# Kernel optimization log

Hardware: AMD Instinct MI355X
Metric: run time of the kernel (lower is better)

The kernel has to match this reference:

```python
import jax, jax.numpy as jnp
import numpy as np

N_NODES = 100000
N_REL = 500
N_EDGES = 600000
DIM = 128


def setup_inputs() -> dict:
    key = jax.random.key(0)
    ks = jax.random.split(key, 10)
    ent = jax.random.normal(ks[0], (N_NODES, DIM), dtype=jnp.float32)
    rel = jax.random.normal(ks[1], (N_REL, DIM), dtype=jnp.float32)
    edge_index = jax.random.randint(ks[2], (2, N_EDGES), 0, N_NODES, dtype=jnp.int64)
    edge_type = jax.random.randint(ks[3], (N_EDGES,), 0, N_REL, dtype=jnp.int64)
    s = 1.0 / np.sqrt(DIM)
    W_self = jax.random.uniform(ks[4], (DIM, DIM), jnp.float32, -s, s)
    b_self = jax.random.uniform(ks[5], (DIM,), jnp.float32, -s, s)
    W_nei = jax.random.uniform(ks[6], (DIM, DIM), jnp.float32, -s, s)
    b_nei = jax.random.uniform(ks[7], (DIM,), jnp.float32, -s, s)
    W_rel = jax.random.uniform(ks[8], (DIM, DIM), jnp.float32, -s, s)
    b_rel = jax.random.uniform(ks[9], (DIM,), jnp.float32, -s, s)
    return {
        "ent": ent, "rel": rel, "edge_index": edge_index, "edge_type": edge_type,
        "W_self": W_self, "b_self": b_self,
        "W_nei": W_nei, "b_nei": b_nei,
        "W_rel": W_rel, "b_rel": b_rel,
    }


def reference(ent, rel, edge_index, edge_type, W_self, b_self, W_nei, b_nei, W_rel, b_rel):
    src, dst = edge_index[0], edge_index[1]
    # gather -> sigmoid-gate -> scatter-add
    msg = ent[src] * jax.nn.sigmoid(rel[edge_type])          # [E, dim]
    agg = jax.ops.segment_sum(msg, dst, num_segments=ent.shape[0])  # [N, dim]
    out_ent = jax.nn.relu(ent @ W_self.T + b_self + agg @ W_nei.T + b_nei)
    out_rel = rel @ W_rel.T + b_rel
    return (out_ent, out_rel)
```

## Files before the change

kernel.cpp:

```cpp
#include <hip/hip_runtime.h>
#include <hip/hip_bf16.h>
#include <math.h>

#define DIM 128

typedef __bf16 bf8 __attribute__((ext_vector_type(8)));
typedef float f4 __attribute__((ext_vector_type(4)));
typedef float f2 __attribute__((ext_vector_type(2)));

struct __align__(8) bf16x4 { __hip_bfloat162 a, b; };

__global__ __launch_bounds__(256) void prep_kernel(
    const float* __restrict__ rel,
    const float* __restrict__ Ws,
    const float* __restrict__ Wn,
    const float* __restrict__ Wr,
    __hip_bfloat16* __restrict__ sigb,
    __hip_bfloat16* __restrict__ Wcat,
    float* __restrict__ Wt_rel,
    int* __restrict__ offs,
    uint2* __restrict__ spack2,
    int nSig, int nSigTot, int sigBlocks, int N, int R,
    int zeroBlocks, int fillQuads) {
    int b = blockIdx.x;
    if (b < sigBlocks) {
        int i = b * 256 + threadIdx.x;
        if (i < nSigTot) {
            float v = 0.f;
            if (i < nSig) {
                float x = rel[i];
                v = 1.0f / (1.0f + expf(-x));
            }
            sigb[i] = __float2bfloat16(v);
        }
    } else if (b < sigBlocks + 32) {
        int idx = (b - sigBlocks) * 256 + threadIdx.x;
        int j  = idx >> 6;
        int k0 = (idx & 63) * 4;
        const float* src = (k0 < DIM) ? &Ws[j * DIM + k0] : &Wn[j * DIM + (k0 - DIM)];
        float4 v = *(const float4*)src;
        bf16x4 o;
        o.a.x = __float2bfloat16(v.x);
        o.a.y = __float2bfloat16(v.y);
        o.b.x = __float2bfloat16(v.z);
        o.b.y = __float2bfloat16(v.w);
        *(bf16x4*)&Wcat[(size_t)j * 256 + k0] = o;
    } else if (b < sigBlocks + 32 + 64) {
        int id = (b - sigBlocks - 32) * 256 + threadIdx.x;
        int k = id >> 7;
        int j = id & 127;
        Wt_rel[id] = Wr[j * DIM + k];
    } else if (b < sigBlocks + 32 + 64 + zeroBlocks) {
        int i = (b - sigBlocks - 32 - 64) * 256 + threadIdx.x;
        if (i <= N) offs[i] = 0;
    } else {
        int i = (b - sigBlocks - 32 - 64 - zeroBlocks) * 256 + threadIdx.x;
        if (i < fillQuads) {
            unsigned gz = (unsigned)R * 256u;
            uint4 s; s.x = 0u; s.y = gz; s.z = 0u; s.w = gz;
            ((uint4*)spack2)[i] = s;
        }
    }
}

__global__ __launch_bounds__(256) void conv_hist_kernel(
    const float* __restrict__ ent,
    __hip_bfloat16* __restrict__ xcat,
    const int* __restrict__ edge_index,
    int* __restrict__ counts,
    int* __restrict__ rank,
    int N, int E, int histBlocks) {
    if ((int)blockIdx.x < histBlocks) {
        int e = blockIdx.x * 256 + threadIdx.x;
        if (e < E) {
            rank[e] = atomicAdd(&counts[edge_index[E + e]], 1);
        }
    } else {
        long long tid = (long long)(blockIdx.x - histBlocks) * 256 + threadIdx.x;
        int row = (int)(tid >> 5);
        int q   = (int)(tid & 31);
        if (row >= N) return;
        float4 v = *(const float4*)&ent[(size_t)row * DIM + q * 4];
        bf16x4 o;
        o.a.x = __float2bfloat16(v.x);
        o.a.y = __float2bfloat16(v.y);
        o.b.x = __float2bfloat16(v.z);
        o.b.y = __float2bfloat16(v.w);
        *(bf16x4*)&xcat[(size_t)row * 256 + q * 4] = o;
    }
}

#define SCAN_TPB 256
#define SCAN_IPT 4
#define SCAN_IPB 1024

__global__ void scan_pass1(int* __restrict__ data,
                           int* __restrict__ blockSums, int N) {
    __shared__ int ts[SCAN_TPB];
    int t = threadIdx.x;
    int base = blockIdx.x * SCAN_IPB + t * SCAN_IPT;
    int v[SCAN_IPT];
    int s = 0;
    #pragma unroll
    for (int i = 0; i < SCAN_IPT; ++i) {
        int idx = base + i;
        int c = (idx < N) ? data[idx] : 0;
        v[i] = (c + 3) & ~3;
        s += v[i];
    }
    ts[t] = s;
    __syncthreads();
    for (int off = 1; off < SCAN_TPB; off <<= 1) {
        int x = (t >= off) ? ts[t - off] : 0;
        __syncthreads();
        ts[t] += x;
        __syncthreads();
    }
    int excl = ts[t] - s;
    #pragma unroll
    for (int i = 0; i < SCAN_IPT; ++i) {
        int idx = base + i;
        if (idx < N) data[idx] = excl;
        excl += v[i];
    }
    if (t == SCAN_TPB - 1) blockSums[blockIdx.x] = ts[t];
}

__global__ __launch_bounds__(256) void scan_finish_kernel(
    int* __restrict__ offs, const int* __restrict__ blockSums,
    int nb, int N) {
    __shared__ int ps[128];
    __shared__ int eps[128];
    int t = threadIdx.x;
    int v = 0;
    if (t < 128) {
        v = (t < nb) ? blockSums[t] : 0;
        ps[t] = v;
    }
    __syncthreads();
    for (int off = 1; off < 128; off <<= 1) {
        int x = (t >= off && t < 128) ? ps[t - off] : 0;
        __syncthreads();
        if (t < 128) ps[t] += x;
        __syncthreads();
    }
    if (t < 128) eps[t] = ps[t] - v;
    __syncthreads();
    int i = blockIdx.x * 256 + t;
    if (i < N)  offs[i] += eps[i >> 10];
    if (i == N) offs[N] = ps[127];
}

__global__ void scatter_ids_kernel(const int* __restrict__ edge_index,
                                   const int* __restrict__ edge_type,
                                   const int* __restrict__ offs,
                                   const int* __restrict__ rank,
                                   uint2* __restrict__ spack2, int E) {
    int e = blockIdx.x * blockDim.x + threadIdx.x;
    if (e >= E) return;
    int dst = edge_index[E + e];
    int p = offs[dst] + rank[e];
    uint2 w;
    w.x = (unsigned)edge_index[e] << 9;
    w.y = (unsigned)edge_type[e] << 8;
    spack2[p] = w;
}

__global__ __launch_bounds__(256) void agg_relout_kernel(
    const __hip_bfloat16* __restrict__ xcat,
    const __hip_bfloat16* __restrict__ sigb,
    const int* __restrict__ offs,
    const uint2* __restrict__ spack2,
    __hip_bfloat16* __restrict__ xcat_w,
    const float* __restrict__ rel,
    const float* __restrict__ Wt_rel,
    const float* __restrict__ b_rel,
    float* __restrict__ out_rel,
    int N, int R, int relBlocks) {
    if ((int)blockIdx.x >= relBlocks) {
        int bid  = blockIdx.x - relBlocks;
        int wid  = bid * 4 + (threadIdx.x >> 6);
        int lane = threadIdx.x & 63;
        if (wid >= N) return;
        int beg = __builtin_amdgcn_readfirstlane(offs[wid]);
        int end = __builtin_amdgcn_readfirstlane(offs[wid + 1]);
        const char* xb = (const char*)xcat;
        const char* gb = (const char*)sigb;
        unsigned so = (unsigned)lane * 4;
        f2 accA = (f2){0.f, 0.f};
        f2 accB = (f2){0.f, 0.f};
        if (beg < end) {
            uint4 q01 = *(const uint4*)(spack2 + beg);
            uint4 q23 = *(const uint4*)(spack2 + beg + 2);
            for (int e = beg; e < end; e += 4) {
                uint4 n01 = *(const uint4*)(spack2 + e + 4);
                uint4 n23 = *(const uint4*)(spack2 + e + 6);
                __hip_bfloat162 v0 = *(const __hip_bfloat162*)(xb + (q01.x + so));
                __hip_bfloat162 g0 = *(const __hip_bfloat162*)(gb + (q01.y + so));
                __hip_bfloat162 v1 = *(const __hip_bfloat162*)(xb + (q01.z + so));
                __hip_bfloat162 g1 = *(const __hip_bfloat162*)(gb + (q01.w + so));
                __hip_bfloat162 v2 = *(const __hip_bfloat162*)(xb + (q23.x + so));
                __hip_bfloat162 g2 = *(const __hip_bfloat162*)(gb + (q23.y + so));
                __hip_bfloat162 v3 = *(const __hip_bfloat162*)(xb + (q23.z + so));
                __hip_bfloat162 g3 = *(const __hip_bfloat162*)(gb + (q23.w + so));
                f2 vf0 = (f2){__bfloat162float(v0.x), __bfloat162float(v0.y)};
                f2 gf0 = (f2){__bfloat162float(g0.x), __bfloat162float(g0.y)};
                f2 vf1 = (f2){__bfloat162float(v1.x), __bfloat162float(v1.y)};
                f2 gf1 = (f2){__bfloat162float(g1.x), __bfloat162float(g1.y)};
                f2 vf2 = (f2){__bfloat162float(v2.x), __bfloat162float(v2.y)};
                f2 gf2 = (f2){__bfloat162float(g2.x), __bfloat162float(g2.y)};
                f2 vf3 = (f2){__bfloat162float(v3.x), __bfloat162float(v3.y)};
                f2 gf3 = (f2){__bfloat162float(g3.x), __bfloat162float(g3.y)};
                accA += vf0 * gf0;
                accB += vf1 * gf1;
                accA += vf2 * gf2;
                accB += vf3 * gf3;
                q01 = n01;
                q23 = n23;
            }
        }
        f2 s = accA + accB;
        __hip_bfloat162 o;
        o.x = __float2bfloat16(s.x);
        o.y = __float2bfloat16(s.y);
        *(__hip_bfloat162*)&xcat_w[(size_t)wid * 256 + 128 + lane * 2] = o;
    } else {
        __shared__ float rr[2][DIM];
        int idx  = blockIdx.x;
        int half = threadIdx.x >> 7;
        int col  = threadIdx.x & 127;
        int row  = idx * 2 + half;
        if (row < R) rr[half][col] = rel[(size_t)row * DIM + col];
        __syncthreads();
        if (row >= R) return;
        float acc = b_rel[col];
        #pragma unroll 8
        for (int k = 0; k < DIM; ++k) {
            acc += rr[half][k] * Wt_rel[k * DIM + col];
        }
        out_rel[(size_t)row * DIM + col] = acc;
    }
}

__global__ __launch_bounds__(256) void gemm_mfma_kernel(
    const __hip_bfloat16* xcat,
    const __hip_bfloat16* __restrict__ Wcat,
    const float* __restrict__ b_self,
    const float* __restrict__ b_nei,
    float* out, int N) {
    __shared__ __hip_bfloat16 Bs[128][264];

    int t    = threadIdx.x;
    int wave = t >> 6;
    int lane = t & 63;
    int quad = lane >> 4;
    int r16  = lane & 15;

    {
        int r = t >> 1, h = t & 1;
        const float4* src = (const float4*)&Wcat[(size_t)r * 256 + h * 128];
        #pragma unroll
        for (int i = 0; i < 16; ++i) {
            *(float4*)&Bs[r][h * 128 + i * 8] = src[i];
        }
    }
    __syncthreads();

    int row0 = blockIdx.x * 128 + wave * 32;

    bf8 x[2][8];
    #pragma unroll
    for (int mt = 0; mt < 2; ++mt) {
        int m = row0 + mt * 16 + r16;
        if (m > N - 1) m = N - 1;
        const __hip_bfloat16* xp = &xcat[(size_t)m * 256 + quad * 8];
        #pragma unroll
        for (int ks = 0; ks < 8; ++ks) {
            x[mt][ks] = *(const bf8*)(xp + ks * 32);
        }
    }

    f4 acc[2][8];
    #pragma unroll
    for (int mt = 0; mt < 2; ++mt)
        #pragma unroll
        for (int jt = 0; jt < 8; ++jt)
            acc[mt][jt] = (f4){0.f, 0.f, 0.f, 0.f};

    #pragma unroll
    for (int ks = 0; ks < 8; ++ks) {
        #pragma unroll
        for (int jt = 0; jt < 8; ++jt) {
            bf8 w = *(const bf8*)&Bs[jt * 16 + r16][ks * 32 + quad * 8];
            acc[0][jt] = __builtin_amdgcn_mfma_f32_16x16x32_bf16(w, x[0][ks], acc[0][jt], 0, 0, 0);
            acc[1][jt] = __builtin_amdgcn_mfma_f32_16x16x32_bf16(w, x[1][ks], acc[1][jt], 0, 0, 0);
        }
    }

    f4 bias4[8];
    #pragma unroll
    for (int jt = 0; jt < 8; ++jt) {
        const float4 bs = *(const float4*)&b_self[jt * 16 + quad * 4];
        const float4 bn = *(const float4*)&b_nei[jt * 16 + quad * 4];
        bias4[jt] = (f4){bs.x + bn.x, bs.y + bn.y, bs.z + bn.z, bs.w + bn.w};
    }

    #pragma unroll
    for (int mt = 0; mt < 2; ++mt) {
        int m = row0 + mt * 16 + r16;
        if (m < N) {
            #pragma unroll
            for (int jt = 0; jt < 8; ++jt) {
                f4 v = acc[mt][jt] + bias4[jt];
                float4 o;
                o.x = fmaxf(v[0], 0.f);
                o.y = fmaxf(v[1], 0.f);
                o.z = fmaxf(v[2], 0.f);
                o.w = fmaxf(v[3], 0.f);
                *(float4*)&out[(size_t)m * DIM + jt * 16 + quad * 4] = o;
            }
        }
    }
}

extern "C" void kernel_launch(void* const* d_in, const int* in_sizes, int n_in,
                              void* d_out, int out_size, void* d_ws, size_t ws_size,
                              hipStream_t stream) {
    const float* ent        = (const float*)d_in[0];
    const float* rel        = (const float*)d_in[1];
    const int*   edge_index = (const int*)d_in[2];
    const int*   edge_type  = (const int*)d_in[3];
    const float* W_self     = (const float*)d_in[4];
    const float* b_self     = (const float*)d_in[5];
    const float* W_nei      = (const float*)d_in[6];
    const float* b_nei      = (const float*)d_in[7];
    const float* W_rel      = (const float*)d_in[8];
    const float* b_rel      = (const float*)d_in[9];

    const int N = in_sizes[0] / DIM;
    const int R = in_sizes[1] / DIM;
    const int E = in_sizes[3];

    float* out     = (float*)d_out;
    float* out_rel = out + (size_t)N * DIM;
    __hip_bfloat16* xcat = (__hip_bfloat16*)d_out;

    __hip_bfloat16* sigb = (__hip_bfloat16*)d_ws;
    float* Wt_rel  = (float*)(sigb + (size_t)(R + 1) * DIM);
    __hip_bfloat16* Wcat = (__hip_bfloat16*)(Wt_rel + DIM * DIM);
    int*   offs    = (int*)(Wcat + 128 * 256);
    int*   bsums   = offs + (N + 8);
    int*   rank    = bsums + 128;
    uint2* spack2  = (uint2*)(rank + E);

    const int nSig = R * DIM;
    const int nSigTot = (R + 1) * DIM;
    const int sigBlocks = (nSigTot + 255) / 256;
    const int zeroBlocks = (N + 1 + 255) / 256;
    const int fillQuads = (E + 3 * N) / 2 + 8;
    const int fillBlocks = (fillQuads + 255) / 256;
    const int scanBlocks = (N + SCAN_IPB - 1) / SCAN_IPB;

    prep_kernel<<<sigBlocks + 32 + 64 + zeroBlocks + fillBlocks, 256, 0, stream>>>(
        rel, W_self, W_nei, W_rel, sigb, Wcat, Wt_rel, offs, spack2,
        nSig, nSigTot, sigBlocks, N, R, zeroBlocks, fillQuads);

    {
        int convBlocks = (int)(((long long)N * 32 + 255) / 256);
        int histBlocks = (E + 255) / 256;
        conv_hist_kernel<<<histBlocks + convBlocks, 256, 0, stream>>>(
            ent, xcat, edge_index, offs, rank, N, E, histBlocks);
    }

    scan_pass1<<<scanBlocks, SCAN_TPB, 0, stream>>>(offs, bsums, N);
    scan_finish_kernel<<<(N + 1 + 255) / 256, 256, 0, stream>>>(
        offs, bsums, scanBlocks, N);

    scatter_ids_kernel<<<(E + 255) / 256, 256, 0, stream>>>(
        edge_index, edge_type, offs, rank, spack2, E);

    {
        int aggBlocks = (int)(((long long)N * 64 + 255) / 256);
        int relBlocks = (R + 1) / 2;
        agg_relout_kernel<<<relBlocks + aggBlocks, 256, 0, stream>>>(
            xcat, sigb, offs, spack2, xcat, rel, Wt_rel, b_rel, out_rel,
            N, R, relBlocks);
    }

    {
        int blocks = (N + 127) / 128;
        gemm_mfma_kernel<<<blocks, 256, 0, stream>>>(xcat, Wcat, b_self, b_nei, out, N);
    }
}
```

Measured before the change: 217.8 us.

## Privatize destination histogram per XCD to avoid cross-die atomic contention

The degree histogram now uses one private count array per XCD, chosen from the hardware XCC_ID register. It uses workgroup-scope relaxed atomics, and each edge's rank carries its XCD id in the top bits. The scan sums the eight per-XCD counts into per-node prefix offsets (pre8), and the scatter adds the matching per-XCD prefix. The aim is to keep atomics in XCD-local L2 instead of paying device-wide coherent atomics. The cost is 8x larger count arrays to zero, read and write, plus an extra random gather in the scatter. It also depends on workgroup-scope atomics being coherent across CUs within one XCD.

```diff
diff --git a/kernel.cpp b/kernel.cpp
--- a/kernel.cpp
+++ b/kernel.cpp
@@ -18,10 +18,10 @@
     __hip_bfloat16* __restrict__ sigb,
     __hip_bfloat16* __restrict__ Wcat,
     float* __restrict__ Wt_rel,
-    int* __restrict__ offs,
     uint2* __restrict__ spack2,
+    int* __restrict__ counts8,
     int nSig, int nSigTot, int sigBlocks, int N, int R,
-    int zeroBlocks, int fillQuads) {
+    int fillQuads, int cntQuads) {
     int b = blockIdx.x;
     if (b < sigBlocks) {
         int i = b * 256 + threadIdx.x;
@@ -50,11 +50,14 @@
         int k = id >> 7;
         int j = id & 127;
         Wt_rel[id] = Wr[j * DIM + k];
-    } else if (b < sigBlocks + 32 + 64 + zeroBlocks) {
+    } else if (b < sigBlocks + 32 + 64 + ((cntQuads + 255) >> 8)) {
         int i = (b - sigBlocks - 32 - 64) * 256 + threadIdx.x;
-        if (i <= N) offs[i] = 0;
+        if (i < cntQuads) {
+            uint4 z; z.x = 0u; z.y = 0u; z.z = 0u; z.w = 0u;
+            ((uint4*)counts8)[i] = z;
+        }
     } else {
-        int i = (b - sigBlocks - 32 - 64 - zeroBlocks) * 256 + threadIdx.x;
+        int i = (b - sigBlocks - 32 - 64 - ((cntQuads + 255) >> 8)) * 256 + threadIdx.x;
         if (i < fillQuads) {
             unsigned gz = (unsigned)R * 256u;
             uint4 s; s.x = 0u; s.y = gz; s.z = 0u; s.w = gz;
@@ -67,13 +70,18 @@
     const float* __restrict__ ent,
     __hip_bfloat16* __restrict__ xcat,
     const int* __restrict__ edge_index,
-    int* __restrict__ counts,
+    int* __restrict__ counts8,
     int* __restrict__ rank,
     int N, int E, int histBlocks) {
     if ((int)blockIdx.x < histBlocks) {
+        int xcd;
+        asm("s_getreg_b32 %0, hwreg(HW_REG_XCC_ID)" : "=s"(xcd));
         int e = blockIdx.x * 256 + threadIdx.x;
         if (e < E) {
-            rank[e] = atomicAdd(&counts[edge_index[E + e]], 1);
+            int d = edge_index[E + e];
+            int lr = __hip_atomic_fetch_add(&counts8[(size_t)xcd * N + d], 1,
+                                            __ATOMIC_RELAXED, __HIP_MEMORY_SCOPE_WORKGROUP);
+            rank[e] = (xcd << 24) | lr;
         }
     } else {
         long long tid = (long long)(blockIdx.x - histBlocks) * 256 + threadIdx.x;
@@ -94,7 +102,9 @@
 #define SCAN_IPT 4
 #define SCAN_IPB 1024
 
-__global__ void scan_pass1(int* __restrict__ data,
+__global__ void scan_pass1(const int* __restrict__ counts8,
+                           int* __restrict__ pre8,
+                           int* __restrict__ offs,
                            int* __restrict__ blockSums, int N) {
     __shared__ int ts[SCAN_TPB];
     int t = threadIdx.x;
@@ -104,7 +114,15 @@
     #pragma unroll
     for (int i = 0; i < SCAN_IPT; ++i) {
         int idx = base + i;
-        int c = (idx < N) ? data[idx] : 0;
+        int c = 0;
+        if (idx < N) {
+            #pragma unroll
+            for (int x = 0; x < 8; ++x) {
+                int cx = counts8[(size_t)x * N + idx];
+                pre8[(size_t)x * N + idx] = c;
+                c += cx;
+            }
+        }
         v[i] = (c + 3) & ~3;
         s += v[i];
     }
@@ -120,7 +138,7 @@
     #pragma unroll
     for (int i = 0; i < SCAN_IPT; ++i) {
         int idx = base + i;
-        if (idx < N) data[idx] = excl;
+        if (idx < N) offs[idx] = excl;
         excl += v[i];
     }
     if (t == SCAN_TPB - 1) blockSums[blockIdx.x] = ts[t];
@@ -154,12 +172,16 @@
 __global__ void scatter_ids_kernel(const int* __restrict__ edge_index,
                                    const int* __restrict__ edge_type,
                                    const int* __restrict__ offs,
+                                   const int* __restrict__ pre8,
                                    const int* __restrict__ rank,
-                                   uint2* __restrict__ spack2, int E) {
+                                   uint2* __restrict__ spack2, int N, int E) {
     int e = blockIdx.x * blockDim.x + threadIdx.x;
     if (e >= E) return;
     int dst = edge_index[E + e];
-    int p = offs[dst] + rank[e];
+    unsigned rk = (unsigned)rank[e];
+    int x  = (int)(rk >> 24);
+    int lr = (int)(rk & 0xFFFFFFu);
+    int p = offs[dst] + pre8[(size_t)x * N + dst] + lr;
     uint2 w;
     w.x = (unsigned)edge_index[e] << 9;
     w.y = (unsigned)edge_type[e] << 8;
@@ -352,32 +374,35 @@
     int*   bsums   = offs + (N + 8);
     int*   rank    = bsums + 128;
     uint2* spack2  = (uint2*)(rank + E);
+    int*   counts8 = (int*)(spack2 + (size_t)(E + 3 * N + 16));
+    int*   pre8    = counts8 + (size_t)8 * N;
 
     const int nSig = R * DIM;
     const int nSigTot = (R + 1) * DIM;
     const int sigBlocks = (nSigTot + 255) / 256;
-    const int zeroBlocks = (N + 1 + 255) / 256;
     const int fillQuads = (E + 3 * N) / 2 + 8;
     const int fillBlocks = (fillQuads + 255) / 256;
+    const int cntQuads = (8 * N) / 4;
+    const int cntBlocks = (cntQuads + 255) / 256;
     const int scanBlocks = (N + SCAN_IPB - 1) / SCAN_IPB;
 
-    prep_kernel<<<sigBlocks + 32 + 64 + zeroBlocks + fillBlocks, 256, 0, stream>>>(
-        rel, W_self, W_nei, W_rel, sigb, Wcat, Wt_rel, offs, spack2,
-        nSig, nSigTot, sigBlocks, N, R, zeroBlocks, fillQuads);
+    prep_kernel<<<sigBlocks + 32 + 64 + cntBlocks + fillBlocks, 256, 0, stream>>>(
+        rel, W_self, W_nei, W_rel, sigb, Wcat, Wt_rel, spack2, counts8,
+        nSig, nSigTot, sigBlocks, N, R, fillQuads, cntQuads);
 
     {
         int convBlocks = (int)(((long long)N * 32 + 255) / 256);
         int histBlocks = (E + 255) / 256;
         conv_hist_kernel<<<histBlocks + convBlocks, 256, 0, stream>>>(
-            ent, xcat, edge_index, offs, rank, N, E, histBlocks);
-    }
-
-    scan_pass1<<<scanBlocks, SCAN_TPB, 0, stream>>>(offs, bsums, N);
+            ent, xcat, edge_index, counts8, rank, N, E, histBlocks);
+    }
+
+    scan_pass1<<<scanBlocks, SCAN_TPB, 0, stream>>>(counts8, pre8, offs, bsums, N);
     scan_finish_kernel<<<(N + 1 + 255) / 256, 256, 0, stream>>>(
         offs, bsums, scanBlocks, N);
 
     scatter_ids_kernel<<<(E + 255) / 256, 256, 0, stream>>>(
-        edge_index, edge_type, offs, rank, spack2, E);
+        edge_index, edge_type, offs, pre8, rank, spack2, N, E);
 
     {
         int aggBlocks = (int)(((long long)N * 64 + 255) / 256);
```

Result: slower. 227.0 us (+4.3%).
